# Performance work log

Measured on AMD Instinct MI355X. Metric: run time of the kernel, lower is better.

## Reference

```python
import jax, jax.numpy as jnp
import numpy as np
import math

N_HEADS = 16
LN_EPS = 1e-5


def _layernorm(x, scale, bias):
    mu = jnp.mean(x, axis=-1, keepdims=True)
    var = jnp.var(x, axis=-1, keepdims=True)
    return (x - mu) * jax.lax.rsqrt(var + LN_EPS) * scale + bias


def _pos_encoding(seq_len, d_model, dtype):
    pos = jnp.arange(seq_len, dtype=jnp.float32)[:, None]
    div = jnp.exp(jnp.arange(0, d_model, 2, dtype=jnp.float32) * (-math.log(10000.0) / d_model))
    pe = jnp.zeros((seq_len, d_model), dtype=jnp.float32)
    pe = pe.at[:, 0::2].set(jnp.sin(pos * div))
    pe = pe.at[:, 1::2].set(jnp.cos(pos * div))
    return pe.astype(dtype)


def setup_inputs() -> dict:
    key = jax.random.key(0)
    ks = jax.random.split(key, 8)
    B, S, V, D, L = 2, 1024, 32000, 1024, 6
    F = 4 * D
    sc = 0.02
    return {
        "tokens": jax.random.randint(ks[0], (B, S), 0, V, dtype=jnp.int32),
        "token_emb": jax.random.normal(ks[1], (V, D), jnp.float32) * sc,
        "Wqkv": jax.random.normal(ks[2], (L, D, 3 * D), jnp.float32) * sc,
        "Wout": jax.random.normal(ks[3], (L, D, D), jnp.float32) * sc,
        "ln1_s": jnp.ones((L, D), jnp.float32),
        "ln1_b": jnp.zeros((L, D), jnp.float32),
        "W1": jax.random.normal(ks[4], (L, D, F), jnp.float32) * sc,
        "b1": jnp.zeros((L, F), jnp.float32),
        "W2": jax.random.normal(ks[5], (L, F, D), jnp.float32) * sc,
        "b2": jnp.zeros((L, D), jnp.float32),
        "ln2_s": jnp.ones((L, D), jnp.float32),
        "ln2_b": jnp.zeros((L, D), jnp.float32),
        "lnf_s": jnp.ones((D,), jnp.float32),
        "lnf_b": jnp.zeros((D,), jnp.float32),
        "Whead": jax.random.normal(ks[6], (D, V), jnp.float32) * sc,
        "bhead": jnp.zeros((V,), jnp.float32),
    }


def _forward(tokens, token_emb, Wqkv, Wout, ln1_s, ln1_b, W1, b1, W2, b2,
             ln2_s, ln2_b, lnf_s, lnf_b, Whead, bhead):
    B, S = tokens.shape
    D = token_emb.shape[1]
    L = Wqkv.shape[0]
    H = N_HEADS
    dk = D // H

    x = token_emb[tokens] + _pos_encoding(S, D, token_emb.dtype)  # [B,S,D]
    causal = jnp.tril(jnp.ones((S, S), dtype=bool))
    neg_inf = jnp.finfo(x.dtype).min

    for l in range(L):
        # --- attention sublayer ---
        h = _layernorm(x, ln1_s[l], ln1_b[l])
        qkv = (h @ Wqkv[l]).reshape(B, S, 3, H, dk)
        q, k, v = jnp.moveaxis(qkv, 2, 0)  # each [B,S,H,dk]
        scores = jnp.einsum('bqhd,bkhd->bhqk', q, k) / math.sqrt(dk)
        scores = jnp.where(causal, scores, neg_inf)
        attn = jax.nn.softmax(scores, axis=-1)  # [B,H,S,S]
        o = jnp.einsum('bhqk,bkhd->bqhd', attn, v).reshape(B, S, D)
        x = x + o @ Wout[l]
        # --- FFN sublayer ---
        h2 = _layernorm(x, ln2_s[l], ln2_b[l])
        x = x + jax.nn.gelu(h2 @ W1[l] + b1[l], approximate=False) @ W2[l] + b2[l]

    x = _layernorm(x, lnf_s, lnf_b)
    return x @ Whead + bhead  # [B,S,V]


def reference(tokens, token_emb, Wqkv, Wout, ln1_s, ln1_b, W1, b1, W2, b2,
              ln2_s, ln2_b, lnf_s, lnf_b, Whead, bhead):
    return _forward(tokens, token_emb, Wqkv, Wout, ln1_s, ln1_b, W1, b1, W2, b2,
                    ln2_s, ln2_b, lnf_s, lnf_b, Whead, bhead)
```

## Files before the change

### kernel.cpp

```cpp
#include <hip/hip_runtime.h>
#include <hip/hip_bf16.h>
#include <math.h>

typedef __bf16 bf16;
typedef __bf16 bf16x4 __attribute__((ext_vector_type(4)));
typedef __bf16 bf16x8 __attribute__((ext_vector_type(8)));
typedef float f32x4 __attribute__((ext_vector_type(4)));

#define GL_AS(p) ((const __attribute__((address_space(1))) void*)(p))
#define LDS_AS(p) ((__attribute__((address_space(3))) void*)(p))

__device__ inline void xcd_remap(int& bm, int& bn, int NBM, int NBN)
{
    const int nwg = NBM * NBN;
    const int flat = bm + NBM * bn;
    const int q = nwg >> 3, r = nwg & 7;
    const int x = flat & 7, i = flat >> 3;
    const int f2 = ((x < r) ? x * (q + 1) : r * (q + 1) + (x - r) * q) + i;
    bm = f2 % NBM;
    bn = f2 / NBM;
}

struct TSeg {
    const float* in; bf16* out; int R, C, nTilesC, tilesPerZ, nTiles;
};

__global__ __launch_bounds__(256) void transpose_all_k(
    TSeg s0, TSeg s1, TSeg s2, TSeg s3, TSeg s4)
{
    int t = blockIdx.x;
    TSeg s;
    if (t < s0.nTiles) s = s0;
    else { t -= s0.nTiles;
    if (t < s1.nTiles) s = s1;
    else { t -= s1.nTiles;
    if (t < s2.nTiles) s = s2;
    else { t -= s2.nTiles;
    if (t < s3.nTiles) s = s3;
    else { t -= s3.nTiles; s = s4; }}}}

    const int z   = t / s.tilesPerZ;
    const int rem = t - z * s.tilesPerZ;
    const int cx  = rem % s.nTilesC, ry = rem / s.nTilesC;

    __shared__ float tl[32][33];
    const int c0 = cx * 32, r0 = ry * 32;
    const size_t zoff = (size_t)z * s.R * s.C;
    const float* inb = s.in + zoff;
    bf16* outb = s.out + zoff;
    const int tx = threadIdx.x, ty = threadIdx.y;
#pragma unroll
    for (int i = 0; i < 32; i += 8)
        tl[ty + i][tx] = inb[(size_t)(r0 + ty + i) * s.C + c0 + tx];
    __syncthreads();
#pragma unroll
    for (int i = 0; i < 32; i += 8)
        outb[(size_t)(c0 + ty + i) * s.R + r0 + tx] = (bf16)tl[tx][ty + i];
}

__global__ __launch_bounds__(256) void embed_k(
    const int* __restrict__ tok, const float* __restrict__ emb,
    float* __restrict__ x)
{
    const int D = 1024;
    const int row = blockIdx.x;
    const int s = row & 1023;
    const int t = tok[row];
    const int d0 = threadIdx.x * 4;
    const float c = 9.210340371976184f / 512.0f;
    const float div0 = expf(-(float)(d0 >> 1) * c);
    const float div1 = expf(-(float)((d0 >> 1) + 1) * c);
    const float a0 = (float)s * div0, a1 = (float)s * div1;
    const f32x4 e = *(const f32x4*)(emb + (size_t)t * D + d0);
    f32x4 o;
    o[0] = e[0] + sinf(a0);
    o[1] = e[1] + cosf(a0);
    o[2] = e[2] + sinf(a1);
    o[3] = e[3] + cosf(a1);
    *(f32x4*)(x + (size_t)row * D + d0) = o;
}

__global__ __launch_bounds__(256) void layernorm_k(
    const float* __restrict__ x, const float* __restrict__ sc,
    const float* __restrict__ bi, bf16* __restrict__ out)
{
    const int D = 1024;
    const int row = blockIdx.x;
    const int d0 = threadIdx.x * 4;
    const f32x4 v = *(const f32x4*)(x + (size_t)row * D + d0);
    float s = v[0] + v[1] + v[2] + v[3];
    float q = v[0] * v[0] + v[1] * v[1] + v[2] * v[2] + v[3] * v[3];
#pragma unroll
    for (int o = 32; o; o >>= 1) { s += __shfl_xor(s, o); q += __shfl_xor(q, o); }
    __shared__ float ls[4], lq[4];
    const int w = threadIdx.x >> 6;
    if ((threadIdx.x & 63) == 0) { ls[w] = s; lq[w] = q; }
    __syncthreads();
    const float S = ls[0] + ls[1] + ls[2] + ls[3];
    const float Q = lq[0] + lq[1] + lq[2] + lq[3];
    const float mu = S * (1.0f / D);
    const float var = Q * (1.0f / D) - mu * mu;
    const float rstd = rsqrtf(var + 1e-5f);
    const f32x4 sc4 = *(const f32x4*)(sc + d0);
    const f32x4 bi4 = *(const f32x4*)(bi + d0);
    bf16x4 o4;
#pragma unroll
    for (int i = 0; i < 4; ++i) o4[i] = (bf16)((v[i] - mu) * rstd * sc4[i] + bi4[i]);
    *(bf16x4*)(out + (size_t)row * D + d0) = o4;
}

template <int EPI, int SK = 1>
__global__ __launch_bounds__(256, 2) void gemm_bt_k(
    const bf16* __restrict__ A, const bf16* __restrict__ Bt,
    float* __restrict__ Cf, bf16* __restrict__ Cb, bf16* __restrict__ Cb2,
    const float* __restrict__ bias, int M, int N, int K)
{
    __shared__ __align__(16) bf16 Al[128 * 64];
    __shared__ __align__(16) bf16 Bl[128 * 64];
    const int tid = threadIdx.x;
    const int l = tid & 63;
    const int wbase = tid & 192;
    const int wr = (tid >> 7) & 1, wc = (tid >> 6) & 1;
    int bm = blockIdx.x, bn = blockIdx.y;
    xcd_remap(bm, bn, gridDim.x, gridDim.y);
    const int kz = blockIdx.z;
    const int Kc = K / SK;

    f32x4 acc[4][4];
#pragma unroll
    for (int i = 0; i < 4; ++i)
#pragma unroll
        for (int j = 0; j < 4; ++j) acc[i][j] = (f32x4){0.f, 0.f, 0.f, 0.f};

    const bf16* Abase = A + (size_t)bm * 128 * K + (size_t)kz * Kc;
    const bf16* Bbase = Bt + (size_t)bn * 128 * K + (size_t)kz * Kc;

    for (int k0 = 0; k0 < Kc; k0 += 64) {
#pragma unroll
        for (int i = 0; i < 4; ++i) {
            const int c = i * 256 + tid;
            const int row = c >> 3, slot = c & 7;
            const int col = ((slot ^ (row & 7)) << 3);
            __builtin_amdgcn_global_load_lds(
                GL_AS(Abase + (size_t)row * K + k0 + col),
                LDS_AS(Al + (i * 256 + wbase) * 8), 16, 0, 0);
        }
#pragma unroll
        for (int i = 0; i < 4; ++i) {
            const int c = i * 256 + tid;
            const int row = c >> 3, slot = c & 7;
            const int col = ((slot ^ (row & 7)) << 3);
            __builtin_amdgcn_global_load_lds(
                GL_AS(Bbase + (size_t)row * K + k0 + col),
                LDS_AS(Bl + (i * 256 + wbase) * 8), 16, 0, 0);
        }
        __syncthreads();

#pragma unroll
        for (int ks = 0; ks < 2; ++ks) {
            bf16x8 af[4], bfr[4];
            const int kb = ks * 64 + ((l >> 4) << 4);
#pragma unroll
            for (int mi = 0; mi < 4; ++mi) {
                const int r = wr * 64 + mi * 16 + (l & 15);
                af[mi] = *(const bf16x8*)((const char*)Al + r * 128 + (kb ^ ((r & 7) << 4)));
            }
#pragma unroll
            for (int ni = 0; ni < 4; ++ni) {
                const int r = wc * 64 + ni * 16 + (l & 15);
                bfr[ni] = *(const bf16x8*)((const char*)Bl + r * 128 + (kb ^ ((r & 7) << 4)));
            }
#pragma unroll
            for (int mi = 0; mi < 4; ++mi)
#pragma unroll
                for (int ni = 0; ni < 4; ++ni)
                    acc[mi][ni] = __builtin_amdgcn_mfma_f32_16x16x32_bf16(
                        af[mi], bfr[ni], acc[mi][ni], 0, 0, 0);
        }
        __syncthreads();
    }

    const int colb = bn * 128 + wc * 64;
    const int rowb = bm * 128 + wr * 64 + ((l >> 4) << 2);
#pragma unroll
    for (int mi = 0; mi < 4; ++mi) {
#pragma unroll
        for (int ni = 0; ni < 4; ++ni) {
            const int col = colb + ni * 16 + (l & 15);
            if constexpr (EPI == 5) {
                const int row0 = rowb + mi * 16;
                if (col < 2048) {
#pragma unroll
                    for (int j = 0; j < 4; ++j)
                        Cb[(size_t)(row0 + j) * N + col] = (bf16)acc[mi][ni][j];
                } else {
                    bf16x4 v4;
#pragma unroll
                    for (int j = 0; j < 4; ++j) v4[j] = (bf16)acc[mi][ni][j];
                    *(bf16x4*)&Cb2[((size_t)(row0 >> 3) * 1024 + (col - 2048)) * 8 + (row0 & 7)] = v4;
                }
            } else {
#pragma unroll
                for (int j = 0; j < 4; ++j) {
                    const int row = rowb + mi * 16 + j;
                    const float v = acc[mi][ni][j];
                    if constexpr (EPI == 0) {
                        Cb[(size_t)row * N + col] = (bf16)v;
                    } else if constexpr (EPI == 1) {
                        if constexpr (SK > 1) atomicAdd(&Cf[(size_t)row * N + col], v);
                        else                  Cf[(size_t)row * N + col] += v;
                    } else if constexpr (EPI == 2) {
                        const float u = v + bias[col];
                        const float g = 0.5f * u * (1.0f + erff(u * 0.70710678118654752f));
                        Cb[(size_t)row * N + col] = (bf16)g;
                    } else if constexpr (EPI == 3) {
                        const float add = (SK == 1 || kz == 0) ? v + bias[col] : v;
                        if constexpr (SK > 1) atomicAdd(&Cf[(size_t)row * N + col], add);
                        else                  Cf[(size_t)row * N + col] += add;
                    } else if constexpr (EPI == 4) {
                        Cf[(size_t)row * N + col] = v + bias[col];
                    }
                }
            }
        }
    }
}

__global__ __launch_bounds__(512, 2) void gemm256_bias_k(
    const bf16* __restrict__ A, const bf16* __restrict__ Bt,
    float* __restrict__ Cf, const float* __restrict__ bias,
    int M, int N, int K)
{
    __shared__ __align__(16) bf16 Al[2][256 * 64];
    __shared__ __align__(16) bf16 Bl[2][256 * 64];
    const int tid = threadIdx.x;
    const int l = tid & 63;
    const int wid = tid >> 6;
    const int wm = wid >> 2, wn = wid & 3;
    const int g = l >> 4, lc = l & 15;
    int bm = blockIdx.x, bn = blockIdx.y;
    xcd_remap(bm, bn, gridDim.x, gridDim.y);

    const bf16* Ab = A + (size_t)bm * 256 * K;
    const bf16* Bb = Bt + (size_t)bn * 256 * K;
    const int NT = K >> 6;

    f32x4 acc[8][4];
#pragma unroll
    for (int i = 0; i < 8; ++i)
#pragma unroll
        for (int j = 0; j < 4; ++j) acc[i][j] = (f32x4){0.f, 0.f, 0.f, 0.f};

    auto stageA = [&](int t, int mh) {
        bf16* dst = Al[t & 1] + mh * 8192;
#pragma unroll
        for (int ld = 0; ld < 2; ++ld) {
            const int c = ld * 512 + tid;
            const int r = c >> 3, slot = c & 7;
            const int col = ((slot ^ (r & 7)) << 3);
            __builtin_amdgcn_global_load_lds(
                GL_AS(Ab + (size_t)(mh * 128 + r) * K + t * 64 + col),
                LDS_AS(dst + (ld * 512 + (tid & 448)) * 8), 16, 0, 0);
        }
    };
    auto stageB = [&](int t, int nh) {
        bf16* dst = Bl[t & 1] + nh * 8192;
#pragma unroll
        for (int ld = 0; ld < 2; ++ld) {
            const int c = ld * 512 + tid;
            const int r = c >> 3, slot = c & 7;
            const int col = ((slot ^ (r & 7)) << 3);
            __builtin_amdgcn_global_load_lds(
                GL_AS(Bb + (size_t)(nh * 128 + r) * K + t * 64 + col),
                LDS_AS(dst + (ld * 512 + (tid & 448)) * 8), 16, 0, 0);
        }
    };
    auto ldA = [&](bf16x8 (&a)[4][2], int mh, int p) {
#pragma unroll
        for (int i = 0; i < 4; ++i) {
            const int r = wm * 128 + mh * 64 + i * 16 + lc;
            const char* base = (const char*)Al[p] + r * 128;
#pragma unroll
            for (int ks = 0; ks < 2; ++ks)
                a[i][ks] = *(const bf16x8*)(base + ((ks * 64 + g * 16) ^ ((r & 7) << 4)));
        }
    };
    auto ldB = [&](bf16x8 (&b)[2][2], int nh, int p) {
#pragma unroll
        for (int i = 0; i < 2; ++i) {
            const int r = wn * 64 + nh * 32 + i * 16 + lc;
            const char* base = (const char*)Bl[p] + r * 128;
#pragma unroll
            for (int ks = 0; ks < 2; ++ks)
                b[i][ks] = *(const bf16x8*)(base + ((ks * 64 + g * 16) ^ ((r & 7) << 4)));
        }
    };
    auto mm = [&](bf16x8 (&a)[4][2], bf16x8 (&b)[2][2], int mh, int nh) {
        __builtin_amdgcn_s_setprio(1);
#pragma unroll
        for (int i = 0; i < 4; ++i)
#pragma unroll
            for (int jn = 0; jn < 2; ++jn) {
                f32x4 ac = acc[mh * 4 + i][nh * 2 + jn];
                ac = __builtin_amdgcn_mfma_f32_16x16x32_bf16(a[i][0], b[jn][0], ac, 0, 0, 0);
                ac = __builtin_amdgcn_mfma_f32_16x16x32_bf16(a[i][1], b[jn][1], ac, 0, 0, 0);
                acc[mh * 4 + i][nh * 2 + jn] = ac;
            }
        __builtin_amdgcn_s_setprio(0);
    };
    auto phase_sync = [&]() {
        __builtin_amdgcn_sched_barrier(0);
        __builtin_amdgcn_s_barrier();
        asm volatile("s_waitcnt lgkmcnt(0)" ::: "memory");
        __builtin_amdgcn_sched_barrier(0);
    };

    stageB(0, 0); stageB(0, 1); stageA(0, 0); stageA(0, 1);
    if (NT > 1) { stageB(1, 0); stageB(1, 1); }
    asm volatile("s_waitcnt vmcnt(4)" ::: "memory");
    __builtin_amdgcn_s_barrier();

    for (int t = 0; t < NT; ++t) {
        const int p = t & 1;
        bf16x8 a[4][2], b0[2][2], b1[2][2];
        ldA(a, 0, p); ldB(b0, 0, p);
        if (t + 1 < NT) stageA(t + 1, 0);
        phase_sync();
        mm(a, b0, 0, 0);
        __builtin_amdgcn_s_barrier();
        ldB(b1, 1, p);
        if (t + 1 < NT) stageA(t + 1, 1);
        phase_sync();
        mm(a, b1, 0, 1);
        __builtin_amdgcn_s_barrier();
        ldA(a, 1, p);
        if (t + 2 < NT) stageB(t + 2, 0);
        phase_sync();
        mm(a, b1, 1, 1);
        __builtin_amdgcn_s_barrier();
        if (t + 2 < NT) stageB(t + 2, 1);
        __builtin_amdgcn_sched_barrier(0);
        if (t + 2 < NT) asm volatile("s_waitcnt vmcnt(4)" ::: "memory");
        else            asm volatile("s_waitcnt vmcnt(0)" ::: "memory");
        __builtin_amdgcn_s_barrier();
        asm volatile("s_waitcnt lgkmcnt(0)" ::: "memory");
        __builtin_amdgcn_sched_barrier(0);
        mm(a, b0, 1, 0);
        __builtin_amdgcn_s_barrier();
    }

    const int colb = bn * 256 + wn * 64;
    const int rowb = bm * 256 + wm * 128 + g * 4;
#pragma unroll
    for (int mi = 0; mi < 8; ++mi) {
#pragma unroll
        for (int ni = 0; ni < 4; ++ni) {
            const int col = colb + ni * 16 + lc;
#pragma unroll
            for (int j = 0; j < 4; ++j) {
                const int row = rowb + mi * 16 + j;
                Cf[(size_t)row * N + col] = acc[mi][ni][j] + bias[col];
            }
        }
    }
}

__global__ __launch_bounds__(256) void attn_mfma_k(
    const bf16* __restrict__ qkv, const bf16* __restrict__ vt,
    bf16* __restrict__ o)
{
    __shared__ __align__(16) bf16 Kl[2][64 * 64];
    __shared__ __align__(16) bf16 Vl[2][64 * 64];
    __shared__ __align__(16) bf16 Pl[4][16][136];

    const int tid = threadIdx.x;
    const int w = tid >> 6, l = tid & 63;
    const int g = l >> 4, lc = l & 15;
    const int qt = blockIdx.x & 15;
    const int bh = blockIdx.x >> 4;
    const int h = bh & 15, b = bh >> 4;
    const int q0 = qt * 64;
    const int qw = q0 + w * 16;
    const int NT = qt + 1;

    const bf16* qbase = qkv + (size_t)b * 1024 * 3072 + h * 64;
    const bf16* kbase = qbase + 1024;
    const bf16* vbase = vt + (size_t)b * 128 * 8192 + h * 512;

    bf16x8 af0, af1;
    {
        const bf16* qp = qbase + (size_t)(qw + lc) * 3072 + g * 8;
        af0 = *(const bf16x8*)qp;
        af1 = *(const bf16x8*)(qp + 32);
    }

    f32x4 acc[4];
#pragma unroll
    for (int dt = 0; dt < 4; ++dt) acc[dt] = (f32x4){0.f, 0.f, 0.f, 0.f};
    f32x4 m  = (f32x4){-1e30f, -1e30f, -1e30f, -1e30f};
    f32x4 ls = (f32x4){0.f, 0.f, 0.f, 0.f};

    auto stage = [&](int t) {
        const int k0 = t * 64;
        const int buf = t & 1;
#pragma unroll
        for (int ld = 0; ld < 2; ++ld) {
            const int c = ld * 256 + tid;
            const int row = c >> 3;
            const int d = (((c & 7) ^ (row & 7)) << 3);
            __builtin_amdgcn_global_load_lds(
                GL_AS(kbase + (size_t)(k0 + row) * 3072 + d),
                LDS_AS(Kl[buf] + (ld * 256 + (tid & 192)) * 8), 16, 0, 0);
        }
#pragma unroll
        for (int ld = 0; ld < 2; ++ld) {
            const int c = ld * 256 + tid;
            const int row = c >> 3;
            const int so = (c & 7) ^ (row & 7);
            __builtin_amdgcn_global_load_lds(
                GL_AS(vbase + (size_t)((k0 >> 3) + so) * 8192 + row * 8),
                LDS_AS(Vl[buf] + (ld * 256 + (tid & 192)) * 8), 16, 0, 0);
        }
    };

    auto compute = [&](int t, bool MASKED) {
        const char* KT = (const char*)Kl[t & 1];
        const char* VT = (const char*)Vl[t & 1];
        const int k0 = t * 64;

        f32x4 s[4];
#pragma unroll
        for (int kt = 0; kt < 4; ++kt) {
            const int r = kt * 16 + lc;
            const bf16x8 kf0 = *(const bf16x8*)(KT + r * 128 + ((g * 16)      ^ ((r & 7) << 4)));
            const bf16x8 kf1 = *(const bf16x8*)(KT + r * 128 + ((64 + g * 16) ^ ((r & 7) << 4)));
            f32x4 sv = (f32x4){0.f, 0.f, 0.f, 0.f};
            sv = __builtin_amdgcn_mfma_f32_16x16x32_bf16(af0, kf0, sv, 0, 0, 0);
            sv = __builtin_amdgcn_mfma_f32_16x16x32_bf16(af1, kf1, sv, 0, 0, 0);
            s[kt] = sv;
        }

#pragma unroll
        for (int kt = 0; kt < 4; ++kt)
#pragma unroll
            for (int j = 0; j < 4; ++j) {
                if (MASKED) {
                    const int row = qw + 4 * g + j;
                    s[kt][j] = (k0 + kt * 16 + lc <= row) ? s[kt][j] * 0.125f : -1e30f;
                } else {
                    s[kt][j] *= 0.125f;
                }
            }

        f32x4 tm;
#pragma unroll
        for (int j = 0; j < 4; ++j)
            tm[j] = fmaxf(fmaxf(s[0][j], s[1][j]), fmaxf(s[2][j], s[3][j]));
#pragma unroll
        for (int off = 8; off; off >>= 1)
#pragma unroll
            for (int j = 0; j < 4; ++j) tm[j] = fmaxf(tm[j], __shfl_xor(tm[j], off));

        f32x4 sc;
#pragma unroll
        for (int j = 0; j < 4; ++j) {
            const float mn = fmaxf(m[j], tm[j]);
            sc[j] = __expf(m[j] - mn);
            m[j] = mn;
        }
        f32x4 p[4];
#pragma unroll
        for (int kt = 0; kt < 4; ++kt)
#pragma unroll
            for (int j = 0; j < 4; ++j) p[kt][j] = __expf(s[kt][j] - m[j]);
#pragma unroll
        for (int j = 0; j < 4; ++j)
            ls[j] = ls[j] * sc[j] + ((p[0][j] + p[1][j]) + (p[2][j] + p[3][j]));
#pragma unroll
        for (int dt = 0; dt < 4; ++dt)
#pragma unroll
            for (int j = 0; j < 4; ++j) acc[dt][j] *= sc[j];

#pragma unroll
        for (int j = 0; j < 4; ++j) {
            const int r = 4 * g + j;
#pragma unroll
            for (int kt = 0; kt < 4; ++kt) {
                const bf16 hi = (bf16)p[kt][j];
                Pl[w][r][kt * 16 + lc]      = hi;
                Pl[w][r][72 + kt * 16 + lc] = (bf16)(p[kt][j] - (float)hi);
            }
        }
        bf16x8 pah[2], pal[2];
#pragma unroll
        for (int ks = 0; ks < 2; ++ks) {
            pah[ks] = *(const bf16x8*)&Pl[w][lc][ks * 32 + g * 8];
            pal[ks] = *(const bf16x8*)&Pl[w][lc][72 + ks * 32 + g * 8];
        }

#pragma unroll
        for (int dt = 0; dt < 4; ++dt) {
            const int r = dt * 16 + lc;
            const bf16x8 vf0 = *(const bf16x8*)(VT + r * 128 + ((g * 16)      ^ ((r & 7) << 4)));
            const bf16x8 vf1 = *(const bf16x8*)(VT + r * 128 + ((64 + g * 16) ^ ((r & 7) << 4)));
            f32x4 a = acc[dt];
            a = __builtin_amdgcn_mfma_f32_16x16x32_bf16(pah[0], vf0, a, 0, 0, 0);
            a = __builtin_amdgcn_mfma_f32_16x16x32_bf16(pah[1], vf1, a, 0, 0, 0);
            a = __builtin_amdgcn_mfma_f32_16x16x32_bf16(pal[0], vf0, a, 0, 0, 0);
            a = __builtin_amdgcn_mfma_f32_16x16x32_bf16(pal[1], vf1, a, 0, 0, 0);
            acc[dt] = a;
        }
    };

    stage(0);
    __syncthreads();
    for (int t = 0; t < NT; ++t) {
        if (t + 1 < NT) stage(t + 1);
        compute(t, t == NT - 1);
        __syncthreads();
    }

    f32x4 inv;
#pragma unroll
    for (int j = 0; j < 4; ++j) {
        float s = ls[j];
#pragma unroll
        for (int off = 8; off; off >>= 1) s += __shfl_xor(s, off);
        inv[j] = 1.0f / s;
    }
    bf16* op = o + (size_t)(b * 1024 + qw) * 1024 + h * 64;
#pragma unroll
    for (int dt = 0; dt < 4; ++dt)
#pragma unroll
        for (int j = 0; j < 4; ++j)
            op[(size_t)(4 * g + j) * 1024 + dt * 16 + lc] = (bf16)(acc[dt][j] * inv[j]);
}

extern "C" void kernel_launch(void* const* d_in, const int* in_sizes, int n_in,
                              void* d_out, int out_size, void* d_ws, size_t ws_size,
                              hipStream_t stream)
{
    const int B = 2, S = 1024, D = 1024, L = 6, F = 4096, V = 32000, H = 16;
    const int M = B * S;

    const int*   tokens    = (const int*)  d_in[0];
    const float* token_emb = (const float*)d_in[1];
    const float* Wqkv      = (const float*)d_in[2];
    const float* Wout      = (const float*)d_in[3];
    const float* ln1_s     = (const float*)d_in[4];
    const float* ln1_b     = (const float*)d_in[5];
    const float* W1        = (const float*)d_in[6];
    const float* b1        = (const float*)d_in[7];
    const float* W2        = (const float*)d_in[8];
    const float* b2        = (const float*)d_in[9];
    const float* ln2_s     = (const float*)d_in[10];
    const float* ln2_b     = (const float*)d_in[11];
    const float* lnf_s     = (const float*)d_in[12];
    const float* lnf_b     = (const float*)d_in[13];
    const float* Whead     = (const float*)d_in[14];
    const float* bhead     = (const float*)d_in[15];
    float* out = (float*)d_out;

    char* w = (char*)d_ws;
    size_t off = 0;
    auto alloc = [&](size_t n) { char* p = w + off; off += (n + 255) & ~(size_t)255; return p; };
    bf16* WqkvT  = (bf16*)alloc((size_t)L * 3 * D * D * 2);
    bf16* WoutT  = (bf16*)alloc((size_t)L * D * D * 2);
    bf16* W1T    = (bf16*)alloc((size_t)L * F * D * 2);
    bf16* W2T    = (bf16*)alloc((size_t)L * D * F * 2);
    bf16* WheadT = (bf16*)alloc((size_t)V * D * 2);
    float* x     = (float*)alloc((size_t)M * D * 4);
    bf16* h      = (bf16*)alloc((size_t)M * D * 2);
    bf16* qkv    = (bf16*)alloc((size_t)M * 3 * D * 2);
    bf16* ob     = (bf16*)alloc((size_t)M * D * 2);
    bf16* mid    = (bf16*)alloc((size_t)M * F * 2);
    bf16* vt     = mid;

    TSeg s0{Wqkv,  WqkvT,  D, 3 * D, 3 * D / 32, (3 * D / 32) * (D / 32), (3 * D / 32) * (D / 32) * L};
    TSeg s1{Wout,  WoutT,  D, D,     D / 32,     (D / 32) * (D / 32),     (D / 32) * (D / 32) * L};
    TSeg s2{W1,    W1T,    D, F,     F / 32,     (F / 32) * (D / 32),     (F / 32) * (D / 32) * L};
    TSeg s3{W2,    W2T,    F, D,     D / 32,     (D / 32) * (F / 32),     (D / 32) * (F / 32) * L};
    TSeg s4{Whead, WheadT, D, V,     V / 32,     (V / 32) * (D / 32),     (V / 32) * (D / 32)};
    const int totTiles = s0.nTiles + s1.nTiles + s2.nTiles + s3.nTiles + s4.nTiles;
    transpose_all_k<<<totTiles, dim3(32, 8), 0, stream>>>(s0, s1, s2, s3, s4);

    embed_k<<<M, 256, 0, stream>>>(tokens, token_emb, x);

    for (int lyr = 0; lyr < L; ++lyr) {
        layernorm_k<<<M, 256, 0, stream>>>(x, ln1_s + lyr * D, ln1_b + lyr * D, h);
        gemm_bt_k<5><<<dim3(M / 128, 3 * D / 128), 256, 0, stream>>>(
            h, WqkvT + (size_t)lyr * 3 * D * D, nullptr, qkv, vt, nullptr, M, 3 * D, D);
        attn_mfma_k<<<B * H * S / 64, 256, 0, stream>>>(qkv, vt, ob);
        gemm_bt_k<1, 4><<<dim3(M / 128, D / 128, 4), 256, 0, stream>>>(
            ob, WoutT + (size_t)lyr * D * D, x, nullptr, nullptr, nullptr, M, D, D);
        layernorm_k<<<M, 256, 0, stream>>>(x, ln2_s + lyr * D, ln2_b + lyr * D, h);
        gemm_bt_k<2><<<dim3(M / 128, F / 128), 256, 0, stream>>>(
            h, W1T + (size_t)lyr * F * D, nullptr, mid, nullptr, b1 + lyr * F, M, F, D);
        gemm_bt_k<3, 4><<<dim3(M / 128, D / 128, 4), 256, 0, stream>>>(
            mid, W2T + (size_t)lyr * D * F, x, nullptr, nullptr, b2 + lyr * D, M, D, F);
    }
    layernorm_k<<<M, 256, 0, stream>>>(x, lnf_s, lnf_b, h);
    gemm256_bias_k<<<dim3(M / 256, V / 256), 512, 0, stream>>>(
        h, WheadT, out, bhead, M, V, D);
}
```

Measured before the change: 1.511 ms.

## Replace head GEMM with 128-tile kernel, halve split-K, balance causal attention

Removes the specialized 256x256 double-buffered head GEMM and runs the vocabulary projection through the generic 128x128 gemm_bt_k without XCD remapping. Split-K for the Wout and W2 projections drops from 4 to 2, which halves the fp32 atomic traffic but gives fewer blocks. Attention reverses the query-tile order for half the batch-head indices so that blocks with short and long causal work interleave. The head change gives up the larger tile's data reuse and its explicit pipelining in exchange for more, smaller blocks.

Result: faster. 1.445 ms (-4.4%).

```diff
diff --git a/kernel.cpp b/kernel.cpp
--- a/kernel.cpp
+++ b/kernel.cpp
@@ -109,7 +109,7 @@
     *(bf16x4*)(out + (size_t)row * D + d0) = o4;
 }
 
-template <int EPI, int SK = 1>
+template <int EPI, int SK = 1, bool SWZ = true>
 __global__ __launch_bounds__(256, 2) void gemm_bt_k(
     const bf16* __restrict__ A, const bf16* __restrict__ Bt,
     float* __restrict__ Cf, bf16* __restrict__ Cb, bf16* __restrict__ Cb2,
@@ -122,7 +122,7 @@
     const int wbase = tid & 192;
     const int wr = (tid >> 7) & 1, wc = (tid >> 6) & 1;
     int bm = blockIdx.x, bn = blockIdx.y;
-    xcd_remap(bm, bn, gridDim.x, gridDim.y);
+    if constexpr (SWZ) xcd_remap(bm, bn, gridDim.x, gridDim.y);
     const int kz = blockIdx.z;
     const int Kc = K / SK;
 
@@ -226,145 +226,6 @@
     }
 }
 
-__global__ __launch_bounds__(512, 2) void gemm256_bias_k(
-    const bf16* __restrict__ A, const bf16* __restrict__ Bt,
-    float* __restrict__ Cf, const float* __restrict__ bias,
-    int M, int N, int K)
-{
-    __shared__ __align__(16) bf16 Al[2][256 * 64];
-    __shared__ __align__(16) bf16 Bl[2][256 * 64];
-    const int tid = threadIdx.x;
-    const int l = tid & 63;
-    const int wid = tid >> 6;
-    const int wm = wid >> 2, wn = wid & 3;
-    const int g = l >> 4, lc = l & 15;
-    int bm = blockIdx.x, bn = blockIdx.y;
-    xcd_remap(bm, bn, gridDim.x, gridDim.y);
-
-    const bf16* Ab = A + (size_t)bm * 256 * K;
-    const bf16* Bb = Bt + (size_t)bn * 256 * K;
-    const int NT = K >> 6;
-
-    f32x4 acc[8][4];
-#pragma unroll
-    for (int i = 0; i < 8; ++i)
-#pragma unroll
-        for (int j = 0; j < 4; ++j) acc[i][j] = (f32x4){0.f, 0.f, 0.f, 0.f};
-
-    auto stageA = [&](int t, int mh) {
-        bf16* dst = Al[t & 1] + mh * 8192;
-#pragma unroll
-        for (int ld = 0; ld < 2; ++ld) {
-            const int c = ld * 512 + tid;
-            const int r = c >> 3, slot = c & 7;
-            const int col = ((slot ^ (r & 7)) << 3);
-            __builtin_amdgcn_global_load_lds(
-                GL_AS(Ab + (size_t)(mh * 128 + r) * K + t * 64 + col),
-                LDS_AS(dst + (ld * 512 + (tid & 448)) * 8), 16, 0, 0);
-        }
-    };
-    auto stageB = [&](int t, int nh) {
-        bf16* dst = Bl[t & 1] + nh * 8192;
-#pragma unroll
-        for (int ld = 0; ld < 2; ++ld) {
-            const int c = ld * 512 + tid;
-            const int r = c >> 3, slot = c & 7;
-            const int col = ((slot ^ (r & 7)) << 3);
-            __builtin_amdgcn_global_load_lds(
-                GL_AS(Bb + (size_t)(nh * 128 + r) * K + t * 64 + col),
-                LDS_AS(dst + (ld * 512 + (tid & 448)) * 8), 16, 0, 0);
-        }
-    };
-    auto ldA = [&](bf16x8 (&a)[4][2], int mh, int p) {
-#pragma unroll
-        for (int i = 0; i < 4; ++i) {
-            const int r = wm * 128 + mh * 64 + i * 16 + lc;
-            const char* base = (const char*)Al[p] + r * 128;
-#pragma unroll
-            for (int ks = 0; ks < 2; ++ks)
-                a[i][ks] = *(const bf16x8*)(base + ((ks * 64 + g * 16) ^ ((r & 7) << 4)));
-        }
-    };
-    auto ldB = [&](bf16x8 (&b)[2][2], int nh, int p) {
-#pragma unroll
-        for (int i = 0; i < 2; ++i) {
-            const int r = wn * 64 + nh * 32 + i * 16 + lc;
-            const char* base = (const char*)Bl[p] + r * 128;
-#pragma unroll
-            for (int ks = 0; ks < 2; ++ks)
-                b[i][ks] = *(const bf16x8*)(base + ((ks * 64 + g * 16) ^ ((r & 7) << 4)));
-        }
-    };
-    auto mm = [&](bf16x8 (&a)[4][2], bf16x8 (&b)[2][2], int mh, int nh) {
-        __builtin_amdgcn_s_setprio(1);
-#pragma unroll
-        for (int i = 0; i < 4; ++i)
-#pragma unroll
-            for (int jn = 0; jn < 2; ++jn) {
-                f32x4 ac = acc[mh * 4 + i][nh * 2 + jn];
-                ac = __builtin_amdgcn_mfma_f32_16x16x32_bf16(a[i][0], b[jn][0], ac, 0, 0, 0);
-                ac = __builtin_amdgcn_mfma_f32_16x16x32_bf16(a[i][1], b[jn][1], ac, 0, 0, 0);
-                acc[mh * 4 + i][nh * 2 + jn] = ac;
-            }
-        __builtin_amdgcn_s_setprio(0);
-    };
-    auto phase_sync = [&]() {
-        __builtin_amdgcn_sched_barrier(0);
-        __builtin_amdgcn_s_barrier();
-        asm volatile("s_waitcnt lgkmcnt(0)" ::: "memory");
-        __builtin_amdgcn_sched_barrier(0);
-    };
-
-    stageB(0, 0); stageB(0, 1); stageA(0, 0); stageA(0, 1);
-    if (NT > 1) { stageB(1, 0); stageB(1, 1); }
-    asm volatile("s_waitcnt vmcnt(4)" ::: "memory");
-    __builtin_amdgcn_s_barrier();
-
-    for (int t = 0; t < NT; ++t) {
-        const int p = t & 1;
-        bf16x8 a[4][2], b0[2][2], b1[2][2];
-        ldA(a, 0, p); ldB(b0, 0, p);
-        if (t + 1 < NT) stageA(t + 1, 0);
-        phase_sync();
-        mm(a, b0, 0, 0);
-        __builtin_amdgcn_s_barrier();
-        ldB(b1, 1, p);
-        if (t + 1 < NT) stageA(t + 1, 1);
-        phase_sync();
-        mm(a, b1, 0, 1);
-        __builtin_amdgcn_s_barrier();
-        ldA(a, 1, p);
-        if (t + 2 < NT) stageB(t + 2, 0);
-        phase_sync();
-        mm(a, b1, 1, 1);
-        __builtin_amdgcn_s_barrier();
-        if (t + 2 < NT) stageB(t + 2, 1);
-        __builtin_amdgcn_sched_barrier(0);
-        if (t + 2 < NT) asm volatile("s_waitcnt vmcnt(4)" ::: "memory");
-        else            asm volatile("s_waitcnt vmcnt(0)" ::: "memory");
-        __builtin_amdgcn_s_barrier();
-        asm volatile("s_waitcnt lgkmcnt(0)" ::: "memory");
-        __builtin_amdgcn_sched_barrier(0);
-        mm(a, b0, 1, 0);
-        __builtin_amdgcn_s_barrier();
-    }
-
-    const int colb = bn * 256 + wn * 64;
-    const int rowb = bm * 256 + wm * 128 + g * 4;
-#pragma unroll
-    for (int mi = 0; mi < 8; ++mi) {
-#pragma unroll
-        for (int ni = 0; ni < 4; ++ni) {
-            const int col = colb + ni * 16 + lc;
-#pragma unroll
-            for (int j = 0; j < 4; ++j) {
-                const int row = rowb + mi * 16 + j;
-                Cf[(size_t)row * N + col] = acc[mi][ni][j] + bias[col];
-            }
-        }
-    }
-}
-
 __global__ __launch_bounds__(256) void attn_mfma_k(
     const bf16* __restrict__ qkv, const bf16* __restrict__ vt,
     bf16* __restrict__ o)
@@ -376,8 +237,9 @@
     const int tid = threadIdx.x;
     const int w = tid >> 6, l = tid & 63;
     const int g = l >> 4, lc = l & 15;
-    const int qt = blockIdx.x & 15;
     const int bh = blockIdx.x >> 4;
+    int qt = blockIdx.x & 15;
+    if (bh & 16) qt = 15 - qt;
     const int h = bh & 15, b = bh >> 4;
     const int q0 = qt * 64;
     const int qw = q0 + w * 16;
@@ -591,15 +453,15 @@
         gemm_bt_k<5><<<dim3(M / 128, 3 * D / 128), 256, 0, stream>>>(
             h, WqkvT + (size_t)lyr * 3 * D * D, nullptr, qkv, vt, nullptr, M, 3 * D, D);
         attn_mfma_k<<<B * H * S / 64, 256, 0, stream>>>(qkv, vt, ob);
-        gemm_bt_k<1, 4><<<dim3(M / 128, D / 128, 4), 256, 0, stream>>>(
+        gemm_bt_k<1, 2><<<dim3(M / 128, D / 128, 2), 256, 0, stream>>>(
             ob, WoutT + (size_t)lyr * D * D, x, nullptr, nullptr, nullptr, M, D, D);
         layernorm_k<<<M, 256, 0, stream>>>(x, ln2_s + lyr * D, ln2_b + lyr * D, h);
         gemm_bt_k<2><<<dim3(M / 128, F / 128), 256, 0, stream>>>(
             h, W1T + (size_t)lyr * F * D, nullptr, mid, nullptr, b1 + lyr * F, M, F, D);
-        gemm_bt_k<3, 4><<<dim3(M / 128, D / 128, 4), 256, 0, stream>>>(
+        gemm_bt_k<3, 2><<<dim3(M / 128, D / 128, 2), 256, 0, stream>>>(
             mid, W2T + (size_t)lyr * D * F, x, nullptr, nullptr, b2 + lyr * D, M, D, F);
     }
     layernorm_k<<<M, 256, 0, stream>>>(x, lnf_s, lnf_b, h);
-    gemm256_bias_k<<<dim3(M / 256, V / 256), 512, 0, stream>>>(
-        h, WheadT, out, bhead, M, V, D);
-}
+    gemm_bt_k<4, 1, false><<<dim3(M / 128, V / 128), 256, 0, stream>>>(
+        h, WheadT, out, nullptr, nullptr, bhead, M, V, D);
+}
```
